# Kernel optimization log

Hardware: AMD Instinct MI355X
Metric: run time of the kernel (lower is better)

## Reference

```python
import jax, jax.numpy as jnp
import numpy as np

H = 64  # hidden_dimension
F = 8   # number_of_input_features
P = 64  # prediction_length
B = 1024
T = 512


def _lstm_cell(x, h, c, Wih, Whh, bih, bhh):
    # PyTorch gate order: input, forget, cell(g), output
    gates = x @ Wih.T + h @ Whh.T + (bih + bhh)  # [B, 4H]
    i, f, g, o = jnp.split(gates, 4, axis=-1)
    c_new = jax.nn.sigmoid(f) * c + jax.nn.sigmoid(i) * jnp.tanh(g)
    h_new = jax.nn.sigmoid(o) * jnp.tanh(c_new)
    return h_new, c_new


def setup_inputs() -> dict:
    key = jax.random.key(0)
    ks = jax.random.split(key, 11)
    s = 1.0 / np.sqrt(H)
    u = lambda k, shape: jax.random.uniform(k, shape, jnp.float32, -s, s)
    return {
        "input_sequence": jax.random.normal(ks[0], (B, T, F), jnp.float32),
        "enc_Wih": u(ks[1], (4 * H, F)),
        "enc_Whh": u(ks[2], (4 * H, H)),
        "enc_bih": u(ks[3], (4 * H,)),
        "enc_bhh": u(ks[4], (4 * H,)),
        "dec_Wih": u(ks[5], (4 * H, F)),
        "dec_Whh": u(ks[6], (4 * H, H)),
        "dec_bih": u(ks[7], (4 * H,)),
        "dec_bhh": u(ks[8], (4 * H,)),
        "fc_W": u(ks[9], (F, H)),
        "fc_b": u(ks[10], (F,)),
    }


def reference(input_sequence, enc_Wih, enc_Whh, enc_bih, enc_bhh,
              dec_Wih, dec_Whh, dec_bih, dec_bhh, fc_W, fc_b):
    Bn = input_sequence.shape[0]
    h0 = jnp.zeros((Bn, H), input_sequence.dtype)
    c0 = jnp.zeros((Bn, H), input_sequence.dtype)

    # ---- Encoder: scan over time ----
    xs = jnp.swapaxes(input_sequence, 0, 1)  # [T, B, F]

    def enc_step(carry, x_t):
        h, c = carry
        h, c = _lstm_cell(x_t, h, c, enc_Wih, enc_Whh, enc_bih, enc_bhh)
        return (h, c), None

    (h, c), _ = jax.lax.scan(enc_step, (h0, c0), xs)

    x_last = input_sequence[:, -1, :]  # [B, F]

    def dec_step(carry, _):
        h, c, x = carry
        h, c = _lstm_cell(x, h, c, dec_Wih, dec_Whh, dec_bih, dec_bhh)
        pred = h @ fc_W.T + fc_b  # [B, F]
        return (h, c, pred), pred

    _, preds = jax.lax.scan(dec_step, (h, c, x_last), None, length=P)
    return jnp.swapaxes(preds, 0, 1)  # [B, P, F]
```

## Files before the change

kernel.cpp:

```cpp
#include <hip/hip_runtime.h>


#define Hh 64
#define Ff 8
#define Tt 512
#define Pp 64
#define BATCH 1024
#define MB 4
#define NBLK (BATCH / MB)
#define ROWS 72
#define ABUF (16 * ROWS + 64)
#define XSTRIDE 32

typedef __attribute__((ext_vector_type(8))) _Float16 half8;
typedef __attribute__((ext_vector_type(4))) _Float16 half4;
typedef __attribute__((ext_vector_type(4))) float f32x4;

#define LOG2E  1.44269504088896340736f
#define K2LOG2 2.88538008177792681472f

__device__ __forceinline__ float sig_pre(float a) {
    return __builtin_amdgcn_rcpf(1.f + __builtin_amdgcn_exp2f(-a));
}
__device__ __forceinline__ float tanh_pre(float a) {
    return 1.f - 2.f * __builtin_amdgcn_rcpf(1.f + __builtin_amdgcn_exp2f(a));
}
__device__ __forceinline__ int arow_base(int m) { return m * ROWS + (m & 3) * 16; }

__device__ __forceinline__ void load_wfrags(
    const float* __restrict__ Whh, const float* __restrict__ Wih,
    int wv, int q, int col, half8 w0[4], half8 w1[4], half8 wx[4])
{
    #pragma unroll
    for (int Tg = 0; Tg < 4; ++Tg) {
        int g = Tg * 64 + wv * 16 + col;
        float sc = (Tg == 2) ? K2LOG2 : LOG2E;
        const float* r0 = Whh + g * 64 + q * 8;
        #pragma unroll
        for (int j = 0; j < 8; ++j) {
            w0[Tg][j] = (_Float16)(r0[j] * sc);
            w1[Tg][j] = (_Float16)(r0[32 + j] * sc);
            wx[Tg][j] = (q == 0) ? (_Float16)(Wih[g * 8 + j] * sc) : (_Float16)0.f;
        }
    }
}

__device__ __forceinline__ void pchain(half8 ax, const half8 wx[4],
                                       const f32x4 biasv[4], f32x4 P[4])
{
    #pragma unroll
    for (int Tg = 0; Tg < 4; ++Tg)
        P[Tg] = __builtin_amdgcn_mfma_f32_16x16x32_f16(ax, wx[Tg], biasv[Tg], 0, 0, 0);
}

__device__ __forceinline__ float qcell(half8 a0, half8 a1,
    const half8 w0[4], const half8 w1[4], const f32x4 P[4], float& cS)
{
    f32x4 Q[4];
    #pragma unroll
    for (int Tg = 0; Tg < 4; ++Tg)
        Q[Tg] = __builtin_amdgcn_mfma_f32_16x16x32_f16(a0, w0[Tg], P[Tg], 0, 0, 0);
    #pragma unroll
    for (int Tg = 0; Tg < 4; ++Tg)
        Q[Tg] = __builtin_amdgcn_mfma_f32_16x16x32_f16(a1, w1[Tg], Q[Tg], 0, 0, 0);
    float si = sig_pre(Q[0][0]);
    float sf = sig_pre(Q[1][0]);
    float tg = tanh_pre(Q[2][0]);
    float so = sig_pre(Q[3][0]);
    cS = sf * cS + si * (K2LOG2 * tg);
    return so * tanh_pre(cS);
}

__global__ __launch_bounds__(256, 1)
void seq2seq_v7(const float* __restrict__ x_seq,
                const float* __restrict__ eWih, const float* __restrict__ eWhh,
                const float* __restrict__ ebih, const float* __restrict__ ebhh,
                const float* __restrict__ dWih, const float* __restrict__ dWhh,
                const float* __restrict__ dbih, const float* __restrict__ dbhh,
                const float* __restrict__ fcW,  const float* __restrict__ fcb,
                float* __restrict__ out)
{
    __shared__ __align__(16) _Float16 xs[(Tt + 2) * XSTRIDE];
    __shared__ __align__(16) _Float16 A0[ABUF];
    __shared__ __align__(16) _Float16 A1[ABUF];
    __shared__ float fcWT[Hh * 9 + 8];
    __shared__ float sfcb[Ff];
    __shared__ __align__(16) _Float16 xdec[MB * Ff];

    const int tid  = threadIdx.x;
    const int wv   = tid >> 6;
    const int lane = tid & 63;
    const int q    = lane >> 4;
    const int col  = lane & 15;
    const int u    = wv * 16 + col;
    const int b0   = blockIdx.x * MB;

    half8 w0[4], w1[4], wx[4];
    load_wfrags(eWhh, eWih, wv, q, col, w0, w1, wx);
    f32x4 biasv[4];
    #pragma unroll
    for (int Tg = 0; Tg < 4; ++Tg) {
        int g = Tg * 64 + u;
        float sc = (Tg == 2) ? K2LOG2 : LOG2E;
        float bv = (ebih[g] + ebhh[g]) * sc;
        biasv[Tg] = (f32x4){bv, bv, bv, bv};
    }

    { int* Z0 = (int*)A0; int* Z1 = (int*)A1;
      for (int i = tid; i < ABUF / 2; i += 256) { Z0[i] = 0; Z1[i] = 0; } }
    for (int i = tid; i < Ff * Hh; i += 256) { int f = i >> 6, uu = i & 63; fcWT[uu * 9 + f] = fcW[i]; }
    if (tid < Ff) sfcb[tid] = fcb[tid];
    if (tid < 32) ((int*)xs)[Tt * 16 + tid] = 0;
    for (int i = tid; i < MB * Tt * 2; i += 256) {
        int b   = i >> 10;
        int rem = i & 1023;
        int t   = rem >> 1;
        int f4  = (rem & 1) * 4;
        const float* src = x_seq + ((size_t)(b0 + b) * Tt + t) * Ff + f4;
        half4 s = { (_Float16)src[0], (_Float16)src[1], (_Float16)src[2], (_Float16)src[3] };
        *(half4*)(&xs[t * XSTRIDE + b * 8 + f4]) = s;
    }
    __syncthreads();

    const _Float16* arA = A0 + arow_base(col) + q * 8;
    const _Float16* arB = A1 + arow_base(col) + q * 8;
    _Float16* hwA = A0 + 4 * q * ROWS + u;
    _Float16* hwB = A1 + 4 * q * ROWS + u;
    const _Float16* xq = xs + (col >> 2) * 8;

    float cS = 0.f;
    f32x4 P[4];
    {   half8 ax = *(const half8*)(xq);
        pchain(ax, wx, biasv, P);
        xq += XSTRIDE; }

    for (int t = 0; t < Tt; t += 2) {
        __syncthreads();
        {
            half8 ax = *(const half8*)(xq); xq += XSTRIDE;
            half8 a0 = *(const half8*)(arA);
            half8 a1 = *(const half8*)(arA + 32);
            float hn = qcell(a0, a1, w0, w1, P, cS);
            *hwB = (_Float16)hn;
            pchain(ax, wx, biasv, P);
        }
        __syncthreads();
        {
            half8 ax = *(const half8*)(xq); xq += XSTRIDE;
            half8 a0 = *(const half8*)(arB);
            half8 a1 = *(const half8*)(arB + 32);
            float hn = qcell(a0, a1, w0, w1, P, cS);
            *hwA = (_Float16)hn;
            pchain(ax, wx, biasv, P);
        }
    }

    load_wfrags(dWhh, dWih, wv, q, col, w0, w1, wx);
    #pragma unroll
    for (int Tg = 0; Tg < 4; ++Tg) {
        int g = Tg * 64 + u;
        float sc = (Tg == 2) ? K2LOG2 : LOG2E;
        float bv = (dbih[g] + dbhh[g]) * sc;
        biasv[Tg] = (f32x4){bv, bv, bv, bv};
    }
    if (tid < MB * Ff) xdec[tid] = xs[(Tt - 1) * XSTRIDE + tid];
    __syncthreads();

    float* predbuf = (float*)xs;
    const _Float16* xdp = xdec + (col >> 2) * 8;

    for (int p = 0; p < Pp; ++p) {
        const _Float16* ar = (p & 1) ? arB : arA;
        _Float16*       hw = (p & 1) ? hwA : hwB;
        const _Float16* hb = (p & 1) ? A0  : A1;
        half8 ax = *(const half8*)(xdp);
        pchain(ax, wx, biasv, P);
        half8 a0 = *(const half8*)(ar);
        half8 a1 = *(const half8*)(ar + 32);
        float hn = qcell(a0, a1, w0, w1, P, cS);
        *hw = (_Float16)hn;
        __syncthreads();
        if (tid < MB * Ff) {
            int b = tid >> 3, f = tid & 7;
            const _Float16* hr = hb + (4 * b) * ROWS;
            float s = sfcb[f];
            #pragma unroll
            for (int ch = 0; ch < 8; ++ch) {
                half8 hh = *(const half8*)(hr + ch * 8);
                #pragma unroll
                for (int j = 0; j < 8; ++j)
                    s += (float)hh[j] * fcWT[(ch * 8 + j) * 9 + f];
            }
            predbuf[b * (Pp * Ff) + p * Ff + f] = s;
            xdec[tid] = (_Float16)s;
        }
        __syncthreads();
    }

    {
        f32x4* out4 = (f32x4*)out + (size_t)b0 * (Pp * Ff / 4);
        const f32x4* pb4 = (const f32x4*)predbuf;
        for (int i = tid; i < MB * Pp * Ff / 4; i += 256)
            out4[i] = pb4[i];
    }
}

extern "C" void kernel_launch(void* const* d_in, const int* in_sizes, int n_in,
                              void* d_out, int out_size, void* d_ws, size_t ws_size,
                              hipStream_t stream) {
    (void)in_sizes; (void)n_in; (void)d_ws; (void)ws_size; (void)out_size;
    hipLaunchKernelGGL(seq2seq_v7, dim3(NBLK), dim3(256), 0, stream,
                       (const float*)d_in[0],
                       (const float*)d_in[1], (const float*)d_in[2],
                       (const float*)d_in[3], (const float*)d_in[4],
                       (const float*)d_in[5], (const float*)d_in[6],
                       (const float*)d_in[7], (const float*)d_in[8],
                       (const float*)d_in[9], (const float*)d_in[10],
                       (float*)d_out);
}
```

Before: 258.6 us.

## Split recurrent MFMA chains and fuse gate activations with shared reciprocals

The two dependent MFMA chains per gate become two independent MFMAs whose results are summed, shortening the serial latency on the recurrent critical path. Sigmoid*tanh products are merged algebraically so each product needs a single reciprocal, and cell state is clamped before exp2 to avoid overflow. The LDS row swizzle for reading h fragments is removed along with its padding, which simplifies addressing but may bring back bank conflicts. Gate g is issued first so its longer tanh path can start earlier.

```diff
diff --git a/kernel.cpp b/kernel.cpp
--- a/kernel.cpp
+++ b/kernel.cpp
@@ -9,7 +9,7 @@
 #define MB 4
 #define NBLK (BATCH / MB)
 #define ROWS 72
-#define ABUF (16 * ROWS + 64)
+#define ABUF (16 * ROWS)
 #define XSTRIDE 32
 
 typedef __attribute__((ext_vector_type(8))) _Float16 half8;
@@ -19,13 +19,8 @@
 #define LOG2E  1.44269504088896340736f
 #define K2LOG2 2.88538008177792681472f
 
-__device__ __forceinline__ float sig_pre(float a) {
-    return __builtin_amdgcn_rcpf(1.f + __builtin_amdgcn_exp2f(-a));
-}
-__device__ __forceinline__ float tanh_pre(float a) {
-    return 1.f - 2.f * __builtin_amdgcn_rcpf(1.f + __builtin_amdgcn_exp2f(a));
-}
-__device__ __forceinline__ int arow_base(int m) { return m * ROWS + (m & 3) * 16; }
+__device__ __forceinline__ float rcp_(float x)  { return __builtin_amdgcn_rcpf(x); }
+__device__ __forceinline__ float exp2_(float x) { return __builtin_amdgcn_exp2f(x); }
 
 __device__ __forceinline__ void load_wfrags(
     const float* __restrict__ Whh, const float* __restrict__ Wih,
@@ -48,37 +43,50 @@
 __device__ __forceinline__ void pchain(half8 ax, const half8 wx[4],
                                        const f32x4 biasv[4], f32x4 P[4])
 {
-    #pragma unroll
-    for (int Tg = 0; Tg < 4; ++Tg)
-        P[Tg] = __builtin_amdgcn_mfma_f32_16x16x32_f16(ax, wx[Tg], biasv[Tg], 0, 0, 0);
+    P[2] = __builtin_amdgcn_mfma_f32_16x16x32_f16(ax, wx[2], biasv[2], 0, 0, 0);
+    P[0] = __builtin_amdgcn_mfma_f32_16x16x32_f16(ax, wx[0], biasv[0], 0, 0, 0);
+    P[1] = __builtin_amdgcn_mfma_f32_16x16x32_f16(ax, wx[1], biasv[1], 0, 0, 0);
+    P[3] = __builtin_amdgcn_mfma_f32_16x16x32_f16(ax, wx[3], biasv[3], 0, 0, 0);
 }
 
 __device__ __forceinline__ float qcell(half8 a0, half8 a1,
     const half8 w0[4], const half8 w1[4], const f32x4 P[4], float& cS)
 {
-    f32x4 Q[4];
-    #pragma unroll
-    for (int Tg = 0; Tg < 4; ++Tg)
-        Q[Tg] = __builtin_amdgcn_mfma_f32_16x16x32_f16(a0, w0[Tg], P[Tg], 0, 0, 0);
-    #pragma unroll
-    for (int Tg = 0; Tg < 4; ++Tg)
-        Q[Tg] = __builtin_amdgcn_mfma_f32_16x16x32_f16(a1, w1[Tg], Q[Tg], 0, 0, 0);
-    float si = sig_pre(Q[0][0]);
-    float sf = sig_pre(Q[1][0]);
-    float tg = tanh_pre(Q[2][0]);
-    float so = sig_pre(Q[3][0]);
-    cS = sf * cS + si * (K2LOG2 * tg);
-    return so * tanh_pre(cS);
+    f32x4 z = {0.f, 0.f, 0.f, 0.f};
+    f32x4 QgA = __builtin_amdgcn_mfma_f32_16x16x32_f16(a0, w0[2], P[2], 0, 0, 0);
+    f32x4 QgB = __builtin_amdgcn_mfma_f32_16x16x32_f16(a1, w1[2], z,    0, 0, 0);
+    f32x4 QiA = __builtin_amdgcn_mfma_f32_16x16x32_f16(a0, w0[0], P[0], 0, 0, 0);
+    f32x4 QiB = __builtin_amdgcn_mfma_f32_16x16x32_f16(a1, w1[0], z,    0, 0, 0);
+    f32x4 QfA = __builtin_amdgcn_mfma_f32_16x16x32_f16(a0, w0[1], P[1], 0, 0, 0);
+    f32x4 QfB = __builtin_amdgcn_mfma_f32_16x16x32_f16(a1, w1[1], z,    0, 0, 0);
+    f32x4 QoA = __builtin_amdgcn_mfma_f32_16x16x32_f16(a0, w0[3], P[3], 0, 0, 0);
+    f32x4 QoB = __builtin_amdgcn_mfma_f32_16x16x32_f16(a1, w1[3], z,    0, 0, 0);
+
+    float Qg = QgA[0] + QgB[0];
+    float Qi = QiA[0] + QiB[0];
+    float Qf = QfA[0] + QfB[0];
+    float Qo = QoA[0] + QoB[0];
+
+    float eg = exp2_(Qg);
+    float ei = exp2_(-Qi);
+    float ef = exp2_(-Qf);
+    float eo = exp2_(-Qo);
+    float it = (eg - 1.f) * rcp_((1.f + ei) * (1.f + eg));
+    float sf = rcp_(1.f + ef);
+    cS = __builtin_fmaf(sf, cS, K2LOG2 * it);
+    float cc = fminf(fmaxf(cS, -80.f), 80.f);
+    float ec = exp2_(cc);
+    return (ec - 1.f) * rcp_((1.f + eo) * (1.f + ec));
 }
 
 __global__ __launch_bounds__(256, 1)
-void seq2seq_v7(const float* __restrict__ x_seq,
-                const float* __restrict__ eWih, const float* __restrict__ eWhh,
-                const float* __restrict__ ebih, const float* __restrict__ ebhh,
-                const float* __restrict__ dWih, const float* __restrict__ dWhh,
-                const float* __restrict__ dbih, const float* __restrict__ dbhh,
-                const float* __restrict__ fcW,  const float* __restrict__ fcb,
-                float* __restrict__ out)
+void seq2seq_v10(const float* __restrict__ x_seq,
+                 const float* __restrict__ eWih, const float* __restrict__ eWhh,
+                 const float* __restrict__ ebih, const float* __restrict__ ebhh,
+                 const float* __restrict__ dWih, const float* __restrict__ dWhh,
+                 const float* __restrict__ dbih, const float* __restrict__ dbhh,
+                 const float* __restrict__ fcW,  const float* __restrict__ fcb,
+                 float* __restrict__ out)
 {
     __shared__ __align__(16) _Float16 xs[(Tt + 2) * XSTRIDE];
     __shared__ __align__(16) _Float16 A0[ABUF];
@@ -122,8 +130,8 @@
     }
     __syncthreads();
 
-    const _Float16* arA = A0 + arow_base(col) + q * 8;
-    const _Float16* arB = A1 + arow_base(col) + q * 8;
+    const _Float16* arA = A0 + col * ROWS + q * 8;
+    const _Float16* arB = A1 + col * ROWS + q * 8;
     _Float16* hwA = A0 + 4 * q * ROWS + u;
     _Float16* hwB = A1 + 4 * q * ROWS + u;
     const _Float16* xq = xs + (col >> 2) * 8;
@@ -209,7 +217,7 @@
                               void* d_out, int out_size, void* d_ws, size_t ws_size,
                               hipStream_t stream) {
     (void)in_sizes; (void)n_in; (void)d_ws; (void)ws_size; (void)out_size;
-    hipLaunchKernelGGL(seq2seq_v7, dim3(NBLK), dim3(256), 0, stream,
+    hipLaunchKernelGGL(seq2seq_v10, dim3(NBLK), dim3(256), 0, stream,
                        (const float*)d_in[0],
                        (const float*)d_in[1], (const float*)d_in[2],
                        (const float*)d_in[3], (const float*)d_in[4],
```

Result: slower. 285.3 us (+10.3%).
